# Performance work log

Measured on AMD Instinct MI355X. Metric: run time of the kernel, lower is better.

Reference implementation:

```python
import jax, jax.numpy as jnp
import numpy as np

EPS_BN = 1e-5
EPS_COS = 1e-8

N, F_IN, HID, OUT, S, NNZ = 50000, 1024, 256, 280, 5000, 800000


def setup_inputs() -> dict:
    key = jax.random.key(0)
    ks = jax.random.split(key, 20)
    inp = {}
    inp["x"] = jax.random.normal(ks[0], (N, F_IN), jnp.float32)
    inp["y"] = jax.random.normal(ks[1], (S, OUT), jnp.float32)
    inp["adj_rows"] = jax.random.randint(ks[2], (NNZ,), 0, N, jnp.int32)
    inp["adj_cols"] = jax.random.randint(ks[3], (NNZ,), 0, N, jnp.int32)
    inp["adj_vals"] = jax.random.uniform(ks[4], (NNZ,), jnp.float32)
    inp["agg_rows"] = jax.random.randint(ks[5], (N,), 0, S, jnp.int32)
    inp["agg_vals"] = jax.random.uniform(ks[6], (N,), jnp.float32)
    inp["perm"] = jax.random.permutation(ks[7], N).astype(jnp.int32)
    # parameters (kaiming-ish scale)
    def lin(k, fi, fo):
        k1, k2 = jax.random.split(k)
        w = jax.random.normal(k1, (fi, fo), jnp.float32) / np.sqrt(fi)
        b = jax.random.normal(k2, (fo,), jnp.float32) * 0.01
        return w, b
    inp["mlp_W"], inp["mlp_b"] = lin(ks[8], F_IN, HID)
    inp["bn_gamma"] = jnp.ones((HID,), jnp.float32)
    inp["bn_beta"] = jnp.zeros((HID,), jnp.float32)
    inp["hg_W1"], inp["hg_b1"] = lin(ks[9], HID, HID)
    inp["hg_W2"], inp["hg_b2"] = lin(ks[10], HID, HID)
    inp["hg_prelu"] = jnp.float32(0.25)
    inp["pred_W"], inp["pred_b"] = lin(ks[11], HID, OUT)
    inp["dgi_W"], inp["dgi_b"] = lin(ks[12], HID, OUT)
    inp["dgi_prelu"] = jnp.float32(0.25)
    return inp


def _spmm(rows, cols, vals, M, n_out):
    # sparse(H) @ M : gather source rows, scale by edge value, scatter-add to dest
    return jax.ops.segment_sum(vals[:, None] * M[cols], rows, num_segments=n_out)


def _prelu(t, a):
    return jnp.where(t >= 0, t, a * t)


def _leaky(t, s):
    return jnp.where(t >= 0, t, s * t)


def reference(x, y, adj_rows, adj_cols, adj_vals, agg_rows, agg_vals, perm,
              mlp_W, mlp_b, bn_gamma, bn_beta, hg_W1, hg_b1, hg_W2, hg_b2,
              hg_prelu, pred_W, pred_b, dgi_W, dgi_b, dgi_prelu):
    n = x.shape[0]
    s = y.shape[0]
    # mlp: Linear -> LeakyReLU(0.1) -> BatchNorm1d (batch stats, training mode)
    h0 = _leaky(x @ mlp_W + mlp_b, 0.1)
    mu = jnp.mean(h0, axis=0)
    var = jnp.mean((h0 - mu) ** 2, axis=0)  # biased, as torch BN training
    h0 = bn_gamma * (h0 - mu) * jax.lax.rsqrt(var + EPS_BN) + bn_beta
    # HGNN, num_layers=2 (dropout = identity in eval)
    t = _spmm(adj_rows, adj_cols, adj_vals, h0 @ hg_W1 + hg_b1, n)
    t = _prelu(t, hg_prelu)
    t = _spmm(adj_rows, adj_cols, adj_vals, t @ hg_W2 + hg_b2, n)
    h = _leaky(t, 0.01)
    x_prime = _leaky(h @ pred_W + pred_b, 0.01)
    # Xenium: loss = MSE(agg_mtx @ x_prime, y); agg_mtx has one nnz per cell
    agg = jax.ops.segment_sum(agg_vals[:, None] * x_prime, agg_rows, num_segments=s)
    loss = jnp.mean((agg - y) ** 2)
    # DGI (1-layer HGNN with PReLU)
    h1 = _prelu(_spmm(adj_rows, adj_cols, adj_vals, h0 @ dgi_W + dgi_b, n), dgi_prelu)
    c = jnp.mean(h1, axis=0)  # (OUT,)
    h2 = _prelu(_spmm(adj_rows, adj_cols, adj_vals, h0[perm] @ dgi_W + dgi_b, n), dgi_prelu)
    c_norm = jnp.linalg.norm(c)
    def cos(hm):
        return (hm @ c) / jnp.maximum(jnp.linalg.norm(hm, axis=1) * c_norm, EPS_COS)
    loss = loss + jnp.mean(1.0 - cos(h1)) + jnp.mean(jnp.maximum(cos(h2), 0.0))
    return (loss, x_prime)
```

## Files before the change

### kernel.cpp

```cpp
#include <hip/hip_runtime.h>
#include <hip/hip_bf16.h>

#define DEVI __device__ __forceinline__

typedef __attribute__((ext_vector_type(8))) short short8;
typedef __attribute__((ext_vector_type(4))) float float4v;

DEVI float bf2f(__hip_bfloat16 v) { return __bfloat162float(v); }
DEVI float ldbs(const ushort* p, size_t i) { return bf2f(((const __hip_bfloat16*)p)[i]); }
DEVI ushort f2bs(float v) {
    __hip_bfloat16 h = __float2bfloat16(v);
    return *(ushort*)&h;
}
DEVI float bfs2f(short s) {
    ushort u = (ushort)s;
    return bf2f(*(__hip_bfloat16*)&u);
}

DEVI float ldin(const void* p, size_t i, int isf32) {
    return isf32 ? ((const float*)p)[i] : bf2f(((const __hip_bfloat16*)p)[i]);
}
DEVI void stio(void* p, size_t i, float v, int isf32) {
    if (isf32) ((float*)p)[i] = v;
    else ((ushort*)p)[i] = f2bs(v);
}

template <int ACT>
DEVI float act_fn(float v, float alpha) {
    if (ACT == 1) return v >= 0.f ? v : 0.1f * v;
    if (ACT == 2) return v >= 0.f ? v : 0.01f * v;
    if (ACT == 3) return v >= 0.f ? v : alpha * v;
    return v;
}

DEVI float waveRed(float v) {
#pragma unroll
    for (int o = 32; o > 0; o >>= 1) v += __shfl_down(v, o);
    return v;
}

DEVI float blockRed(float v) {
    __shared__ float sm[16];
    int lane = threadIdx.x & 63, w = threadIdx.x >> 6;
    v = waveRed(v);
    if (lane == 0) sm[w] = v;
    __syncthreads();
    if (w == 0) {
        int nw = (blockDim.x + 63) >> 6;
        v = (lane < nw) ? sm[lane] : 0.f;
        v = waveRed(v);
    }
    return v;
}

__global__ void probe_k(const void* __restrict__ x, int* __restrict__ flag) {
    __shared__ int sfails;
    int t = threadIdx.x;
    if (t == 0) sfails = 0;
    __syncthreads();
    const __hip_bfloat16* xb = (const __hip_bfloat16*)x;
    int my = 0;
    for (int i = t; i < 4096; i += 256) {
        float v = bf2f(xb[i]);
        float a = fabsf(v);
        if (!(a <= 64.f) || (v != 0.f && a < 1e-6f)) my++;
    }
    atomicAdd(&sfails, my);
    __syncthreads();
    if (t == 0) flag[0] = (sfails > 409) ? 1 : 0;
}

struct Cvt5 {
    const void* src[5];
    ushort* dst[5];
    int K[5];
    int N[5];
};
__global__ void cvt_all_k(Cvt5 d, const int* __restrict__ flagp) {
    int f32 = flagp[0];
    int seg = blockIdx.y;
    int idx = blockIdx.x * blockDim.x + threadIdx.x;
    int K = d.K[seg], Nc = d.N[seg];
    int total = K * Nc;
    if (idx < total) {
        int k = idx / Nc, n = idx % Nc;
        d.dst[seg][(size_t)n * K + k] = f2bs(ldin(d.src[seg], idx, f32));
    }
}

#define TP 40
template <int AMODE, int ACT, int OMODE, int BMODE>
__global__ __launch_bounds__(256) void mgemm_k(
    const void* __restrict__ A, const ushort* __restrict__ Bt,
    const void* __restrict__ bias, const float* __restrict__ rsc,
    const void* __restrict__ alpha_p, void* __restrict__ outp, ushort* __restrict__ outp2,
    const int* __restrict__ flagp, int M, int K, int Nc, int LDo) {
    __shared__ short As[128 * TP];
    __shared__ short Bs[128 * TP];
    const int f32 = flagp[0];
    const int tid = threadIdx.x;
    const int lane = tid & 63;
    const int l15 = lane & 15;
    const int quad = lane >> 4;
    const int wid = tid >> 6;
    const int mW = (wid >> 1) * 64;
    const int nW = (wid & 1) * 64;
    const int mBase = blockIdx.y * 128;
    const int nBase = blockIdx.x * 128;

    float4v acc[4][4];
#pragma unroll
    for (int i = 0; i < 4; i++)
#pragma unroll
        for (int j = 0; j < 4; j++) acc[i][j] = (float4v){0.f, 0.f, 0.f, 0.f};

    short8 sa[2], sb[2];
    float4v fa[2][2];

    auto issue_tile = [&](int k0) {
#pragma unroll
        for (int i = 0; i < 2; i++) {
            int chunk = i * 256 + tid;
            int row = chunk >> 2;
            int c = chunk & 3;
            int gr = mBase + row;
            int gn = nBase + row;
            size_t geA = (size_t)gr * K + k0 + c * 8;
            if (AMODE == 0 && f32) {
                if (gr < M) {
                    const float* af = (const float*)A + geA;
                    fa[i][0] = *(const float4v*)af;
                    fa[i][1] = *(const float4v*)(af + 4);
                } else {
                    fa[i][0] = (float4v){0.f, 0.f, 0.f, 0.f};
                    fa[i][1] = (float4v){0.f, 0.f, 0.f, 0.f};
                }
            } else {
                sa[i] = (gr < M) ? *(const short8*)((const ushort*)A + geA)
                                 : (short8){0, 0, 0, 0, 0, 0, 0, 0};
            }
            sb[i] = (gn < Nc) ? *(const short8*)(Bt + (size_t)gn * K + k0 + c * 8)
                              : (short8){0, 0, 0, 0, 0, 0, 0, 0};
        }
    };

    auto commit_tile = [&]() {
#pragma unroll
        for (int i = 0; i < 2; i++) {
            int chunk = i * 256 + tid;
            int row = chunk >> 2;
            int c = chunk & 3;
            short8 va;
            if (AMODE == 0 && f32) {
#pragma unroll
                for (int j = 0; j < 4; j++) va[j] = (short)f2bs(fa[i][0][j]);
#pragma unroll
                for (int j = 0; j < 4; j++) va[4 + j] = (short)f2bs(fa[i][1][j]);
            } else {
                va = sa[i];
            }
            *(short8*)&As[row * TP + c * 8] = va;
            *(short8*)&Bs[row * TP + c * 8] = sb[i];
        }
    };

    const int nk = K >> 5;
    issue_tile(0);
    for (int t = 0; t < nk; ++t) {
        __syncthreads();
        commit_tile();
        if (t + 1 < nk) issue_tile((t + 1) << 5);
        __syncthreads();

        short8 af[4], bf[4];
#pragma unroll
        for (int i = 0; i < 4; i++)
            af[i] = *(const short8*)&As[(mW + i * 16 + l15) * TP + quad * 8];
#pragma unroll
        for (int j = 0; j < 4; j++)
            bf[j] = *(const short8*)&Bs[(nW + j * 16 + l15) * TP + quad * 8];
#pragma unroll
        for (int i = 0; i < 4; i++)
#pragma unroll
            for (int j = 0; j < 4; j++)
                acc[i][j] =
                    __builtin_amdgcn_mfma_f32_16x16x32_bf16(af[i], bf[j], acc[i][j], 0, 0, 0);
    }

    const float alpha = (ACT == 3) ? ldin(alpha_p, 0, f32) : 0.f;
#pragma unroll
    for (int i = 0; i < 4; i++) {
#pragma unroll
        for (int j = 0; j < 4; j++) {
            int gcn = nBase + nW + j * 16 + l15;
            if (gcn >= Nc) continue;
            float bv = ldin(bias, gcn, f32);
#pragma unroll
            for (int r = 0; r < 4; r++) {
                int grm = mBase + mW + i * 16 + quad * 4 + r;
                if (grm >= M) continue;
                float be = (BMODE == 1) ? rsc[grm] * bv : bv;
                float v = act_fn<ACT>(acc[i][j][r] + be, alpha);
                if (OMODE == 1) {
                    stio(outp, 1 + (size_t)grm * Nc + gcn, v, f32);
                    outp2[(size_t)grm * LDo + gcn] = f2bs(v);
                } else {
                    ((ushort*)outp)[(size_t)grm * LDo + gcn] = f2bs(v);
                }
            }
        }
    }
}

__global__ void count_k(const int* __restrict__ rows, int* __restrict__ counts, int nnz) {
    int i = blockIdx.x * blockDim.x + threadIdx.x;
    if (i < nnz) atomicAdd(&counts[rows[i]], 1);
}

__global__ __launch_bounds__(1024) void scan_local_k(const int* __restrict__ counts,
                                                     int* __restrict__ offs,
                                                     int* __restrict__ bsums, int n) {
    __shared__ int sm[1024];
    int t = threadIdx.x;
    int g = blockIdx.x * 1024 + t;
    int v = (g < n) ? counts[g] : 0;
    sm[t] = v;
    __syncthreads();
    for (int d = 1; d < 1024; d <<= 1) {
        int add = (t >= d) ? sm[t - d] : 0;
        __syncthreads();
        sm[t] += add;
        __syncthreads();
    }
    if (g < n) offs[g] = sm[t] - v;
    if (t == 1023) bsums[blockIdx.x] = sm[t];
}

__global__ void scan_bsums_k(int* bsums, int nb) {
    if (threadIdx.x == 0 && blockIdx.x == 0) {
        int acc = 0;
        for (int i = 0; i < nb; i++) {
            int v = bsums[i];
            bsums[i] = acc;
            acc += v;
        }
    }
}

__global__ void scan_add_k(int* __restrict__ offs, const int* __restrict__ bsums, int n, int nnz) {
    int g = blockIdx.x * blockDim.x + threadIdx.x;
    if (g < n) offs[g] += bsums[g >> 10];
    if (g == 0) offs[n] = nnz;
}

__global__ void fill_k(const int* __restrict__ rows, const int* __restrict__ cols,
                       const void* __restrict__ vals, const int* __restrict__ perm,
                       const int* __restrict__ offs, int* __restrict__ cursor,
                       int* __restrict__ cols_s, int* __restrict__ colsp_s,
                       float* __restrict__ vals_s, float* __restrict__ rsum,
                       const int* __restrict__ flagp, int nnz) {
    int e = blockIdx.x * blockDim.x + threadIdx.x;
    if (e < nnz) {
        int r = rows[e];
        int pos = offs[r] + atomicAdd(&cursor[r], 1);
        int c = cols[e];
        float v = ldin(vals, e, flagp[0]);
        cols_s[pos] = c;
        colsp_s[pos] = perm[c];
        vals_s[pos] = v;
        atomicAdd(&rsum[r], v);
    }
}

__global__ void fill_s_k(const int* __restrict__ rows, const void* __restrict__ vals,
                         const int* __restrict__ offs, int* __restrict__ cursor,
                         int* __restrict__ idx_s, float* __restrict__ val_s,
                         const int* __restrict__ flagp, int n) {
    int e = blockIdx.x * blockDim.x + threadIdx.x;
    if (e < n) {
        int r = rows[e];
        int pos = offs[r] + atomicAdd(&cursor[r], 1);
        idx_s[pos] = e;
        val_s[pos] = ldin(vals, e, flagp[0]);
    }
}

template <int ACT, bool DUAL, int EPI>
__global__ __launch_bounds__(256) void spmmv_k(
    const int* __restrict__ offs, const int* __restrict__ cols_s,
    const int* __restrict__ colsp_s, const float* __restrict__ vals_s,
    const void* __restrict__ alpha_p, const int* __restrict__ flagp,
    const ushort* __restrict__ Min, ushort* __restrict__ out1, ushort* __restrict__ out2,
    const float* __restrict__ scale, const float* __restrict__ shift,
    const float* __restrict__ rsum, int Nrow) {
    const int LD = 256;
    int row = blockIdx.x * 4 + (threadIdx.x >> 6);
    if (row >= Nrow) return;
    int lane = threadIdx.x & 63;
    int half = lane >> 5, l5 = lane & 31;
    int sbase = l5 * 8;
    float alpha = (ACT == 3) ? ldin(alpha_p, 0, flagp[0]) : 0.f;
    int s = offs[row], e = offs[row + 1];
    float a[8] = {}, b[8] = {};

    constexpr int DEPTH = 4;
    int i = s + half;
    for (; i + 2 * (DEPTH - 1) < e; i += 2 * DEPTH) {
        int c[DEPTH];
        float v[DEPTH];
        int cp[DEPTH];
#pragma unroll
        for (int u = 0; u < DEPTH; u++) {
            c[u] = cols_s[i + 2 * u];
            v[u] = vals_s[i + 2 * u];
        }
        if (DUAL) {
#pragma unroll
            for (int u = 0; u < DEPTH; u++) cp[u] = colsp_s[i + 2 * u];
        }
        short8 hv[DEPTH], gv[DEPTH];
#pragma unroll
        for (int u = 0; u < DEPTH; u++) {
            hv[u] = *(const short8*)(Min + (size_t)c[u] * LD + sbase);
            if (DUAL) gv[u] = *(const short8*)(Min + (size_t)cp[u] * LD + sbase);
        }
#pragma unroll
        for (int u = 0; u < DEPTH; u++) {
#pragma unroll
            for (int j = 0; j < 8; j++) a[j] += v[u] * bfs2f(hv[u][j]);
            if (DUAL) {
#pragma unroll
                for (int j = 0; j < 8; j++) b[j] += v[u] * bfs2f(gv[u][j]);
            }
        }
    }
    for (; i < e; i += 2) {
        float v = vals_s[i];
        int c = cols_s[i];
        short8 h = *(const short8*)(Min + (size_t)c * LD + sbase);
#pragma unroll
        for (int j = 0; j < 8; j++) a[j] += v * bfs2f(h[j]);
        if (DUAL) {
            int cp = colsp_s[i];
            short8 g = *(const short8*)(Min + (size_t)cp * LD + sbase);
#pragma unroll
            for (int j = 0; j < 8; j++) b[j] += v * bfs2f(g[j]);
        }
    }
#pragma unroll
    for (int j = 0; j < 8; j++) {
        a[j] += __shfl_xor(a[j], 32);
        if (DUAL) b[j] += __shfl_xor(b[j], 32);
    }
    if (half == 0) {
        size_t obase = (size_t)row * LD + sbase;
        short8 o;
        if (EPI == 1) {
            float4v sc0 = *(const float4v*)(scale + sbase);
            float4v sc1 = *(const float4v*)(scale + sbase + 4);
            float4v sh0 = *(const float4v*)(shift + sbase);
            float4v sh1 = *(const float4v*)(shift + sbase + 4);
            float rr = rsum[row];
#pragma unroll
            for (int j = 0; j < 4; j++) o[j] = (short)f2bs(sc0[j] * a[j] + rr * sh0[j]);
#pragma unroll
            for (int j = 0; j < 4; j++) o[4 + j] = (short)f2bs(sc1[j] * a[4 + j] + rr * sh1[j]);
            *(short8*)(out1 + obase) = o;
            if (DUAL) {
#pragma unroll
                for (int j = 0; j < 4; j++) o[j] = (short)f2bs(sc0[j] * b[j] + rr * sh0[j]);
#pragma unroll
                for (int j = 0; j < 4; j++)
                    o[4 + j] = (short)f2bs(sc1[j] * b[4 + j] + rr * sh1[j]);
                *(short8*)(out2 + obase) = o;
            }
        } else {
#pragma unroll
            for (int j = 0; j < 8; j++) o[j] = (short)f2bs(act_fn<ACT>(a[j], alpha));
            *(short8*)(out1 + obase) = o;
            if (DUAL) {
#pragma unroll
                for (int j = 0; j < 8; j++) o[j] = (short)f2bs(act_fn<ACT>(b[j], alpha));
                *(short8*)(out2 + obase) = o;
            }
        }
    }
}

__global__ __launch_bounds__(256) void aggmse_k(
    const int* __restrict__ soffs, const int* __restrict__ sidx, const float* __restrict__ sval,
    const ushort* __restrict__ xp, const void* __restrict__ y, const int* __restrict__ flagp,
    float* __restrict__ lacc, int S, int F, int LDxp) {
    int srow = blockIdx.x * 4 + (threadIdx.x >> 6);
    int lane = threadIdx.x & 63;
    int half = lane >> 5, l5 = lane & 31;
    int FC = F >> 3;
    bool has1 = (l5 + 32) < FC;
    float a0[8] = {}, a1[8] = {};
    if (srow < S) {
        int s = soffs[srow], e = soffs[srow + 1];
        constexpr int DEPTH = 4;
        int i = s + half;
        for (; i + 2 * (DEPTH - 1) < e; i += 2 * DEPTH) {
            int n[DEPTH];
            float v[DEPTH];
#pragma unroll
            for (int u = 0; u < DEPTH; u++) {
                n[u] = sidx[i + 2 * u];
                v[u] = sval[i + 2 * u];
            }
            short8 h0v[DEPTH], h1v[DEPTH];
#pragma unroll
            for (int u = 0; u < DEPTH; u++) {
                const ushort* src = xp + (size_t)n[u] * LDxp;
                h0v[u] = *(const short8*)(src + l5 * 8);
                if (has1) h1v[u] = *(const short8*)(src + (l5 + 32) * 8);
            }
#pragma unroll
            for (int u = 0; u < DEPTH; u++) {
#pragma unroll
                for (int j = 0; j < 8; j++) a0[j] += v[u] * bfs2f(h0v[u][j]);
                if (has1) {
#pragma unroll
                    for (int j = 0; j < 8; j++) a1[j] += v[u] * bfs2f(h1v[u][j]);
                }
            }
        }
        for (; i < e; i += 2) {
            float v = sval[i];
            int n = sidx[i];
            const ushort* src = xp + (size_t)n * LDxp;
            short8 h = *(const short8*)(src + l5 * 8);
#pragma unroll
            for (int j = 0; j < 8; j++) a0[j] += v * bfs2f(h[j]);
            if (has1) {
                short8 h2 = *(const short8*)(src + (l5 + 32) * 8);
#pragma unroll
                for (int j = 0; j < 8; j++) a1[j] += v * bfs2f(h2[j]);
            }
        }
    }
#pragma unroll
    for (int j = 0; j < 8; j++) {
        a0[j] += __shfl_xor(a0[j], 32);
        if (has1) a1[j] += __shfl_xor(a1[j], 32);
    }
    float ss = 0.f;
    if (srow < S && half == 0) {
        int f32 = flagp[0];
        size_t base = (size_t)srow * F;
#pragma unroll
        for (int j = 0; j < 8; j++) {
            float d = a0[j] - ldin(y, base + l5 * 8 + j, f32);
            ss += d * d;
        }
        if (has1) {
#pragma unroll
            for (int j = 0; j < 8; j++) {
                float d = a1[j] - ldin(y, base + (l5 + 32) * 8 + j, f32);
                ss += d * d;
            }
        }
    }
    ss = blockRed(ss);
    if (threadIdx.x == 0) atomicAdd(&lacc[0], ss);
}

__global__ __launch_bounds__(256) void bn_stats_k(const ushort* __restrict__ h,
                                                  float* __restrict__ sum,
                                                  float* __restrict__ sumsq, int nrows, int rpb) {
    int c = threadIdx.x;
    int rs = blockIdx.x * rpb;
    int re = min(rs + rpb, nrows);
    float s = 0.f, s2 = 0.f;
    int H = blockDim.x;
    for (int r = rs; r < re; r++) {
        float v = ldbs(h, (size_t)r * H + c);
        s += v;
        s2 += v * v;
    }
    atomicAdd(&sum[c], s);
    atomicAdd(&sumsq[c], s2);
}

__global__ void bn_final_k(const float* __restrict__ sum, const float* __restrict__ sumsq,
                           const void* __restrict__ gamma, const void* __restrict__ beta,
                           float* __restrict__ scale, float* __restrict__ shift,
                           const int* __restrict__ flagp, int nrows) {
    int c = threadIdx.x;
    int f32 = flagp[0];
    float mu = sum[c] / nrows;
    float var = sumsq[c] / nrows - mu * mu;
    float sc = ldin(gamma, c, f32) * rsqrtf(var + 1e-5f);
    scale[c] = sc;
    shift[c] = ldin(beta, c, f32) - mu * sc;
}

__global__ __launch_bounds__(320) void colsum_k(const ushort* __restrict__ h,
                                                float* __restrict__ accum, int nrows, int F,
                                                int rpb) {
    int f = threadIdx.x;
    if (f >= F) return;
    int rs = blockIdx.x * rpb;
    int re = min(rs + rpb, nrows);
    float s = 0.f;
    for (int r = rs; r < re; r++) s += ldbs(h, (size_t)r * F + f);
    atomicAdd(&accum[f], s);
}

__global__ __launch_bounds__(320) void cfinal_k(const float* __restrict__ accum,
                                                float* __restrict__ c, float* __restrict__ cnorm,
                                                int N, int F) {
    int f = threadIdx.x;
    float v = 0.f;
    if (f < F) {
        v = accum[f] / N;
        c[f] = v;
    }
    float s2 = blockRed(v * v);
    if (threadIdx.x == 0) cnorm[0] = sqrtf(s2);
}

template <int MODE>
__global__ __launch_bounds__(256) void cos_k(const ushort* __restrict__ h,
                                             const float* __restrict__ c,
                                             const float* __restrict__ cnorm,
                                             float* __restrict__ acc, int N, int F) {
    int gw = (blockIdx.x * blockDim.x + threadIdx.x) >> 6;
    int lane = threadIdx.x & 63;
    int nw = (gridDim.x * blockDim.x) >> 6;
    float cn = cnorm[0];
    float s = 0.f;
    for (int row = gw; row < N; row += nw) {
        float dot = 0.f, nsq = 0.f;
        for (int f = lane; f < F; f += 64) {
            float v = ldbs(h, (size_t)row * F + f);
            dot += v * c[f];
            nsq += v * v;
        }
#pragma unroll
        for (int o = 32; o > 0; o >>= 1) {
            dot += __shfl_down(dot, o);
            nsq += __shfl_down(nsq, o);
        }
        if (lane == 0) {
            float cosv = dot / fmaxf(sqrtf(nsq) * cn, 1e-8f);
            s += (MODE == 1) ? fmaxf(cosv, 0.f) : cosv;
        }
    }
    s = blockRed(s);
    if (threadIdx.x == 0) atomicAdd(acc, s);
}

__global__ void final_k(const float* __restrict__ lacc, void* __restrict__ dout,
                        const int* __restrict__ flagp, int SOUT, int N) {
    if (threadIdx.x == 0 && blockIdx.x == 0) {
        float loss = lacc[0] / SOUT + (1.f - lacc[1] / N) + lacc[2] / N;
        stio(dout, 0, loss, flagp[0]);
    }
}

extern "C" void kernel_launch(void* const* d_in, const int* in_sizes, int n_in,
                              void* d_out, int out_size, void* d_ws, size_t ws_size,
                              hipStream_t stream) {
    const void* x = d_in[0];
    const void* y = d_in[1];
    const int* adj_rows = (const int*)d_in[2];
    const int* adj_cols = (const int*)d_in[3];
    const void* adj_vals = d_in[4];
    const int* agg_rows = (const int*)d_in[5];
    const void* agg_vals = d_in[6];
    const int* perm = (const int*)d_in[7];
    const void* mlp_W = d_in[8];
    const void* mlp_b = d_in[9];
    const void* bn_gamma = d_in[10];
    const void* bn_beta = d_in[11];
    const void* hg_W1 = d_in[12];
    const void* hg_b1 = d_in[13];
    const void* hg_W2 = d_in[14];
    const void* hg_b2 = d_in[15];
    const void* hg_prelu = d_in[16];
    const void* pred_W = d_in[17];
    const void* pred_b = d_in[18];
    const void* dgi_W = d_in[19];
    const void* dgi_b = d_in[20];
    const void* dgi_prelu = d_in[21];

    const int N = in_sizes[5];
    const int NNZ = in_sizes[2];
    const int F_IN = in_sizes[0] / N;
    const int HID = in_sizes[9];
    const int OUT = in_sizes[18];
    const int S = in_sizes[1] / OUT;

    const int LDP = (OUT + 63) & ~63;

    char* w = (char*)d_ws;
    size_t off = 0;
    auto alloc = [&](size_t b) -> char* {
        char* p = w + off;
        off += (b + 255) & ~(size_t)255;
        return p;
    };
    ushort* h0_bf = (ushort*)alloc((size_t)N * HID * 2);
    ushort* U_bf = (ushort*)alloc((size_t)N * HID * 2);
    ushort* Up_bf = (ushort*)alloc((size_t)N * HID * 2);
    ushort* zA_bf = (ushort*)alloc((size_t)N * LDP * 2);
    ushort* zB_bf = (ushort*)alloc((size_t)N * LDP * 2);
    ushort* h2_bf = (ushort*)alloc((size_t)N * OUT * 2);
    ushort* xp_ws = zA_bf;
    ushort* mlpWt = (ushort*)alloc((size_t)HID * F_IN * 2);
    ushort* hgW1t = (ushort*)alloc((size_t)HID * HID * 2);
    ushort* hgW2t = (ushort*)alloc((size_t)HID * HID * 2);
    ushort* predWt = (ushort*)alloc((size_t)OUT * HID * 2);
    ushort* dgiWt = (ushort*)alloc((size_t)OUT * HID * 2);
    int* offs = (int*)alloc((size_t)(N + 1) * 4);
    int nbscan = (N + 1023) / 1024;
    int* bsums = (int*)alloc((size_t)nbscan * 4);
    int* cols_s = (int*)alloc((size_t)NNZ * 4);
    int* colsp_s = (int*)alloc((size_t)NNZ * 4);
    float* vals_s = (float*)alloc((size_t)NNZ * 4);
    int* soffs = (int*)alloc((size_t)(S + 1) * 4);
    int nbscan_s = (S + 1023) / 1024;
    int* sbsums = (int*)alloc((size_t)nbscan_s * 4);
    int* sidx = (int*)alloc((size_t)N * 4);
    float* sval = (float*)alloc((size_t)N * 4);
    float* bn_scale = (float*)alloc((size_t)HID * 4);
    float* bn_shift = (float*)alloc((size_t)HID * 4);
    float* c_vec = (float*)alloc((size_t)OUT * 4);
    float* cnorm = (float*)alloc(4);
    int* dflag = (int*)alloc(16);
    char* zero_base = w + off;
    int* counts = (int*)alloc((size_t)N * 4);
    int* cursor = (int*)alloc((size_t)N * 4);
    int* scnt = (int*)alloc((size_t)S * 4);
    int* scursor = (int*)alloc((size_t)S * 4);
    float* rsum = (float*)alloc((size_t)N * 4);
    float* bn_sum = (float*)alloc((size_t)HID * 4);
    float* bn_sumsq = (float*)alloc((size_t)HID * 4);
    float* c_acc = (float*)alloc((size_t)OUT * 4);
    float* lacc = (float*)alloc(16);
    size_t zero_bytes = (w + off) - zero_base;
    hipMemsetAsync(zero_base, 0, zero_bytes, stream);

    probe_k<<<1, 256, 0, stream>>>(x, dflag);

    Cvt5 cv;
    cv.src[0] = mlp_W;  cv.dst[0] = mlpWt;  cv.K[0] = F_IN; cv.N[0] = HID;
    cv.src[1] = hg_W1;  cv.dst[1] = hgW1t;  cv.K[1] = HID;  cv.N[1] = HID;
    cv.src[2] = hg_W2;  cv.dst[2] = hgW2t;  cv.K[2] = HID;  cv.N[2] = HID;
    cv.src[3] = pred_W; cv.dst[3] = predWt; cv.K[3] = HID;  cv.N[3] = OUT;
    cv.src[4] = dgi_W;  cv.dst[4] = dgiWt;  cv.K[4] = HID;  cv.N[4] = OUT;
    cvt_all_k<<<dim3((F_IN * HID + 255) / 256, 5), 256, 0, stream>>>(cv, dflag);

    count_k<<<(NNZ + 255) / 256, 256, 0, stream>>>(adj_rows, counts, NNZ);
    scan_local_k<<<nbscan, 1024, 0, stream>>>(counts, offs, bsums, N);
    scan_bsums_k<<<1, 64, 0, stream>>>(bsums, nbscan);
    scan_add_k<<<(N + 255) / 256, 256, 0, stream>>>(offs, bsums, N, NNZ);
    fill_k<<<(NNZ + 255) / 256, 256, 0, stream>>>(adj_rows, adj_cols, adj_vals, perm, offs,
                                                  cursor, cols_s, colsp_s, vals_s, rsum, dflag,
                                                  NNZ);
    count_k<<<(N + 255) / 256, 256, 0, stream>>>(agg_rows, scnt, N);
    scan_local_k<<<nbscan_s, 1024, 0, stream>>>(scnt, soffs, sbsums, S);
    scan_bsums_k<<<1, 64, 0, stream>>>(sbsums, nbscan_s);
    scan_add_k<<<(S + 255) / 256, 256, 0, stream>>>(soffs, sbsums, S, N);
    fill_s_k<<<(N + 255) / 256, 256, 0, stream>>>(agg_rows, agg_vals, soffs, scursor, sidx, sval,
                                                  dflag, N);

    const int MT = (N + 127) / 128;
    const int NT_H = (HID + 127) / 128;
    const int NT_O = (OUT + 127) / 128;
    const int SPB = (N + 3) / 4;

    mgemm_k<0, 1, 0, 0><<<dim3(NT_H, MT), 256, 0, stream>>>(
        x, mlpWt, mlp_b, nullptr, nullptr, h0_bf, nullptr, dflag, N, F_IN, HID, HID);
    bn_stats_k<<<(N + 127) / 128, HID, 0, stream>>>(h0_bf, bn_sum, bn_sumsq, N, 128);
    bn_final_k<<<1, HID, 0, stream>>>(bn_sum, bn_sumsq, bn_gamma, bn_beta, bn_scale, bn_shift,
                                      dflag, N);

    spmmv_k<0, true, 1><<<SPB, 256, 0, stream>>>(offs, cols_s, colsp_s, vals_s, nullptr, dflag,
                                                 h0_bf, U_bf, Up_bf, bn_scale, bn_shift, rsum, N);

    mgemm_k<1, 3, 0, 1><<<dim3(NT_H, MT), 256, 0, stream>>>(
        U_bf, hgW1t, hg_b1, rsum, hg_prelu, zB_bf, nullptr, dflag, N, HID, HID, HID);
    mgemm_k<1, 0, 0, 0><<<dim3(NT_H, MT), 256, 0, stream>>>(
        zB_bf, hgW2t, hg_b2, nullptr, nullptr, zA_bf, nullptr, dflag, N, HID, HID, HID);
    spmmv_k<2, false, 0><<<SPB, 256, 0, stream>>>(offs, cols_s, nullptr, vals_s, nullptr, dflag,
                                                  zA_bf, zB_bf, nullptr, nullptr, nullptr,
                                                  nullptr, N);

    mgemm_k<1, 2, 1, 0><<<dim3(NT_O, MT), 256, 0, stream>>>(
        zB_bf, predWt, pred_b, nullptr, nullptr, d_out, xp_ws, dflag, N, HID, OUT, LDP);
    aggmse_k<<<(S + 3) / 4, 256, 0, stream>>>(soffs, sidx, sval, xp_ws, y, dflag, lacc, S, OUT,
                                              LDP);

    mgemm_k<1, 3, 0, 1><<<dim3(NT_O, MT), 256, 0, stream>>>(
        U_bf, dgiWt, dgi_b, rsum, dgi_prelu, zB_bf, nullptr, dflag, N, HID, OUT, OUT);
    mgemm_k<1, 3, 0, 1><<<dim3(NT_O, MT), 256, 0, stream>>>(
        Up_bf, dgiWt, dgi_b, rsum, dgi_prelu, h2_bf, nullptr, dflag, N, HID, OUT, OUT);

    colsum_k<<<(N + 127) / 128, 320, 0, stream>>>(zB_bf, c_acc, N, OUT, 128);
    cfinal_k<<<1, 320, 0, stream>>>(c_acc, c_vec, cnorm, N, OUT);
    cos_k<0><<<256, 256, 0, stream>>>(zB_bf, c_vec, cnorm, &lacc[1], N, OUT);
    cos_k<1><<<256, 256, 0, stream>>>(h2_bf, c_vec, cnorm, &lacc[2], N, OUT);

    final_k<<<1, 64, 0, stream>>>(lacc, d_out, dflag, S * OUT, N);
}
```

Baseline: 1.201 ms.

## Double-buffer LDS tiles in MFMA GEMM with two-deep register prefetch

Rewrites the GEMM main loop to use two LDS buffers and two register staging sets, so global loads for tile t+2 are issued before computing on tile t, and only one barrier is used per k-step instead of two. Custom barriers wait only on LDS counters, so global loads can stay in flight across the barrier. This doubles LDS use per block and adds staging registers, which may lower occupancy.

New measurement: 1.279 ms. 6.5% more time.

```diff
diff --git a/kernel.cpp b/kernel.cpp
--- a/kernel.cpp
+++ b/kernel.cpp
@@ -89,14 +89,84 @@
 }
 
 #define TP 40
+
+#define LBAR()                                                 \
+    do {                                                       \
+        asm volatile("s_waitcnt lgkmcnt(0)" ::: "memory");     \
+        __builtin_amdgcn_s_barrier();                          \
+    } while (0)
+
+#define ISSUE(SET, K0)                                                            \
+    do {                                                                          \
+        int kk = (K0);                                                            \
+        _Pragma("unroll") for (int ii = 0; ii < 2; ii++) {                        \
+            int chunk = ii * 256 + tid;                                           \
+            int row = chunk >> 2;                                                 \
+            int cc = chunk & 3;                                                   \
+            int gr = mBase + row;                                                 \
+            int gn = nBase + row;                                                 \
+            size_t geA = (size_t)gr * K + kk + cc * 8;                            \
+            if (AMODE == 0 && f32) {                                              \
+                if (gr < M) {                                                     \
+                    const float* af = (const float*)A + geA;                      \
+                    fs##SET[ii][0] = *(const float4v*)af;                         \
+                    fs##SET[ii][1] = *(const float4v*)(af + 4);                   \
+                } else {                                                          \
+                    fs##SET[ii][0] = (float4v){0.f, 0.f, 0.f, 0.f};               \
+                    fs##SET[ii][1] = (float4v){0.f, 0.f, 0.f, 0.f};               \
+                }                                                                 \
+            } else {                                                              \
+                fs##SET[ii][0] =                                                  \
+                    (gr < M) ? *(const float4v*)((const ushort*)A + geA)          \
+                             : (float4v){0.f, 0.f, 0.f, 0.f};                     \
+            }                                                                     \
+            sb##SET[ii] = (gn < Nc)                                               \
+                              ? *(const short8*)(Bt + (size_t)gn * K + kk + cc * 8) \
+                              : (short8){0, 0, 0, 0, 0, 0, 0, 0};                 \
+        }                                                                         \
+    } while (0)
+
+#define COMMIT(SET, BUF)                                                          \
+    do {                                                                          \
+        _Pragma("unroll") for (int ii = 0; ii < 2; ii++) {                        \
+            int chunk = ii * 256 + tid;                                           \
+            int row = chunk >> 2;                                                 \
+            int cc = chunk & 3;                                                   \
+            short8 va;                                                            \
+            if (AMODE == 0 && f32) {                                              \
+                _Pragma("unroll") for (int jj = 0; jj < 4; jj++)                  \
+                    va[jj] = (short)f2bs(fs##SET[ii][0][jj]);                     \
+                _Pragma("unroll") for (int jj = 0; jj < 4; jj++)                  \
+                    va[4 + jj] = (short)f2bs(fs##SET[ii][1][jj]);                 \
+            } else {                                                              \
+                va = __builtin_bit_cast(short8, fs##SET[ii][0]);                  \
+            }                                                                     \
+            *(short8*)&As[BUF][row * TP + cc * 8] = va;                           \
+            *(short8*)&Bs[BUF][row * TP + cc * 8] = sb##SET[ii];                  \
+        }                                                                         \
+    } while (0)
+
+#define COMPUTE(BUF)                                                              \
+    do {                                                                          \
+        short8 af[4], bf[4];                                                      \
+        _Pragma("unroll") for (int ii = 0; ii < 4; ii++)                          \
+            af[ii] = *(const short8*)&As[BUF][(mW + ii * 16 + l15) * TP + quad * 8]; \
+        _Pragma("unroll") for (int jj = 0; jj < 4; jj++)                          \
+            bf[jj] = *(const short8*)&Bs[BUF][(nW + jj * 16 + l15) * TP + quad * 8]; \
+        _Pragma("unroll") for (int ii = 0; ii < 4; ii++)                          \
+            _Pragma("unroll") for (int jj = 0; jj < 4; jj++)                      \
+                acc[ii][jj] = __builtin_amdgcn_mfma_f32_16x16x32_bf16(             \
+                    af[ii], bf[jj], acc[ii][jj], 0, 0, 0);                        \
+    } while (0)
+
 template <int AMODE, int ACT, int OMODE, int BMODE>
 __global__ __launch_bounds__(256) void mgemm_k(
     const void* __restrict__ A, const ushort* __restrict__ Bt,
     const void* __restrict__ bias, const float* __restrict__ rsc,
     const void* __restrict__ alpha_p, void* __restrict__ outp, ushort* __restrict__ outp2,
     const int* __restrict__ flagp, int M, int K, int Nc, int LDo) {
-    __shared__ short As[128 * TP];
-    __shared__ short Bs[128 * TP];
+    __shared__ short As[2][128 * TP];
+    __shared__ short Bs[2][128 * TP];
     const int f32 = flagp[0];
     const int tid = threadIdx.x;
     const int lane = tid & 63;
@@ -114,77 +184,25 @@
 #pragma unroll
         for (int j = 0; j < 4; j++) acc[i][j] = (float4v){0.f, 0.f, 0.f, 0.f};
 
-    short8 sa[2], sb[2];
-    float4v fa[2][2];
-
-    auto issue_tile = [&](int k0) {
-#pragma unroll
-        for (int i = 0; i < 2; i++) {
-            int chunk = i * 256 + tid;
-            int row = chunk >> 2;
-            int c = chunk & 3;
-            int gr = mBase + row;
-            int gn = nBase + row;
-            size_t geA = (size_t)gr * K + k0 + c * 8;
-            if (AMODE == 0 && f32) {
-                if (gr < M) {
-                    const float* af = (const float*)A + geA;
-                    fa[i][0] = *(const float4v*)af;
-                    fa[i][1] = *(const float4v*)(af + 4);
-                } else {
-                    fa[i][0] = (float4v){0.f, 0.f, 0.f, 0.f};
-                    fa[i][1] = (float4v){0.f, 0.f, 0.f, 0.f};
-                }
-            } else {
-                sa[i] = (gr < M) ? *(const short8*)((const ushort*)A + geA)
-                                 : (short8){0, 0, 0, 0, 0, 0, 0, 0};
-            }
-            sb[i] = (gn < Nc) ? *(const short8*)(Bt + (size_t)gn * K + k0 + c * 8)
-                              : (short8){0, 0, 0, 0, 0, 0, 0, 0};
-        }
-    };
-
-    auto commit_tile = [&]() {
-#pragma unroll
-        for (int i = 0; i < 2; i++) {
-            int chunk = i * 256 + tid;
-            int row = chunk >> 2;
-            int c = chunk & 3;
-            short8 va;
-            if (AMODE == 0 && f32) {
-#pragma unroll
-                for (int j = 0; j < 4; j++) va[j] = (short)f2bs(fa[i][0][j]);
-#pragma unroll
-                for (int j = 0; j < 4; j++) va[4 + j] = (short)f2bs(fa[i][1][j]);
-            } else {
-                va = sa[i];
-            }
-            *(short8*)&As[row * TP + c * 8] = va;
-            *(short8*)&Bs[row * TP + c * 8] = sb[i];
-        }
-    };
+    float4v fs0[2][2], fs1[2][2];
+    short8 sb0[2], sb1[2];
 
     const int nk = K >> 5;
-    issue_tile(0);
-    for (int t = 0; t < nk; ++t) {
-        __syncthreads();
-        commit_tile();
-        if (t + 1 < nk) issue_tile((t + 1) << 5);
-        __syncthreads();
-
-        short8 af[4], bf[4];
-#pragma unroll
-        for (int i = 0; i < 4; i++)
-            af[i] = *(const short8*)&As[(mW + i * 16 + l15) * TP + quad * 8];
-#pragma unroll
-        for (int j = 0; j < 4; j++)
-            bf[j] = *(const short8*)&Bs[(nW + j * 16 + l15) * TP + quad * 8];
-#pragma unroll
-        for (int i = 0; i < 4; i++)
-#pragma unroll
-            for (int j = 0; j < 4; j++)
-                acc[i][j] =
-                    __builtin_amdgcn_mfma_f32_16x16x32_bf16(af[i], bf[j], acc[i][j], 0, 0, 0);
+    ISSUE(0, 0);
+    if (nk > 1) ISSUE(1, 32);
+    COMMIT(0, 0);
+    LBAR();
+    for (int t = 0; t < nk; t += 2) {
+        if (t + 2 < nk) ISSUE(0, (t + 2) << 5);
+        COMPUTE(0);
+        if (t + 1 < nk) COMMIT(1, 1);
+        LBAR();
+        if (t + 1 < nk) {
+            if (t + 3 < nk) ISSUE(1, (t + 3) << 5);
+            COMPUTE(1);
+            if (t + 2 < nk) COMMIT(0, 0);
+            LBAR();
+        }
     }
 
     const float alpha = (ACT == 3) ? ldin(alpha_p, 0, f32) : 0.f;
```
